# Optimization experiments

Measured on AMD Instinct MI355X. Metric: run time of the kernel, lower is better.

The kernel has to match this reference:

```python
import jax, jax.numpy as jnp
import numpy as np

D_IN = 768      # residual-stream width
D_SAE = 16384   # dictionary size
T = 4           # positions per window
K = 64          # TopK sparsity
PREFIX = (8192, 16384)  # prefix_sum for n_scales=2 even split
B = 1024


def setup_inputs() -> dict:
    key = jax.random.key(0)
    ks = jax.random.split(key, 6)
    x = jax.random.normal(ks[0], (B, T, D_IN), jnp.float32)
    # encoder weight ~ kaiming-uniform scale
    W_enc = jax.random.normal(ks[1], (T, D_IN, D_SAE), jnp.float32) * (1.0 / np.sqrt(D_IN))
    b_enc = jnp.zeros((D_SAE,), jnp.float32)
    # per-scale decoders, row-normalized over (T, d_in) as in _normalize_decoder
    def make_dec(k, prefix):
        W = jax.random.normal(k, (prefix, T, D_IN), jnp.float32)
        norms = jnp.linalg.norm(W.reshape(prefix, -1), axis=1).clip(1e-8)
        return W / norms[:, None, None]
    W_dec0 = make_dec(ks[2], PREFIX[0])
    W_dec1 = make_dec(ks[3], PREFIX[1])
    b_dec0 = jnp.zeros((T, D_IN), jnp.float32)
    b_dec1 = jnp.zeros((T, D_IN), jnp.float32)
    # non-identity per-position prefix permutation (T, d_sae)
    perm_keys = jax.random.split(ks[4], T)
    pos_prefix_perm = jax.vmap(lambda k: jax.random.permutation(k, D_SAE))(perm_keys).astype(jnp.int32)
    return {
        'x': x, 'W_enc': W_enc, 'b_enc': b_enc,
        'W_dec0': W_dec0, 'b_dec0': b_dec0,
        'W_dec1': W_dec1, 'b_dec1': b_dec1,
        'pos_prefix_perm': pos_prefix_perm,
    }


def reference(x, W_enc, b_enc, W_dec0, b_dec0, W_dec1, b_dec1, pos_prefix_perm):
    # ---- encode: pre-activation + per-row TopK + ReLU scatter into sparse code z
    pre = jnp.einsum('btd,tds->bs', x, W_enc) + b_enc            # (B, d_sae)
    vals, idx = jax.lax.top_k(pre, K)                            # (B, K)
    b = pre.shape[0]
    z = jnp.zeros_like(pre).at[jnp.arange(b)[:, None], idx].set(jax.nn.relu(vals))
    # ---- matryoshka per-(position, scale) reconstruction loss
    total = jnp.asarray(0.0, pre.dtype)
    x_hat_full = None
    for W, bd in ((W_dec0, b_dec0), (W_dec1, b_dec1)):
        prefix = W.shape[0]
        # position-dependent permutation gather: z_g[b,t,p] = z[b, perm[t,p]]
        z_g = z[:, pos_prefix_perm[:, :prefix]]                  # (B, T, prefix)
        x_hat = jnp.einsum('btp,ptd->btd', z_g, W) + bd          # (B, T, d_in)
        # sum over t of mean_b sum_d err^2  (== loop over t in the original)
        total = total + jnp.sum(jnp.mean(jnp.sum((x_hat - x) ** 2, axis=-1), axis=0))
        x_hat_full = x_hat
    total = total / (T * 2)  # divide by T * n_scales
    # aux-k loss: freshly initialized module has no dead latents
    # (num_tokens_since_fired starts at 0 << dead_threshold_tokens), so l_auxk == 0.
    return total, x_hat_full, z
```

## Files before the change

### kernel.cpp

```cpp
#include <hip/hip_runtime.h>
#include <hip/hip_bf16.h>
#include <stdint.h>

#define NB    1024
#define NT    4
#define NDIN  768
#define NSAE  16384
#define NK    64
#define KDIM  3072
#define PFX0  8192
#define KT96  96
#define VKD   6144

typedef _Float16 f16x8 __attribute__((ext_vector_type(8)));
typedef _Float16 f16x4 __attribute__((ext_vector_type(4)));
typedef float    f32x4 __attribute__((ext_vector_type(4)));

__device__ __forceinline__ unsigned f2key(float f) {
    union { float f; unsigned u; } cv; cv.f = f;
    unsigned u = cv.u;
    return u ^ ((unsigned)((int)u >> 31) | 0x80000000u);
}

__device__ __forceinline__ void ld16(const void* g, void* l) {
    __builtin_amdgcn_global_load_lds(
        (const __attribute__((address_space(1))) void*)g,
        (__attribute__((address_space(3))) void*)l, 16, 0, 0);
}

__global__ __launch_bounds__(256) void conv_a_kernel(
    const float* __restrict__ A, _Float16* __restrict__ A2)
{
    const int gid = blockIdx.x * 256 + threadIdx.x;
    const int m = gid / (KDIM / 4);
    const int k = (gid % (KDIM / 4)) * 4;
    const float4 v = *(const float4*)(A + (size_t)m * KDIM + k);
    const float vv[4] = { v.x, v.y, v.z, v.w };
    f16x4 h, l;
#pragma unroll
    for (int j = 0; j < 4; ++j) {
        const float sv = vv[j] * 64.f;
        const _Float16 hh = (_Float16)sv;
        h[j] = hh;
        l[j] = (_Float16)(sv - (float)hh);
    }
    const size_t ob = (size_t)m * VKD + (k >> 5) * 64 + (k & 31);
    *(f16x4*)(A2 + ob)      = h;
    *(f16x4*)(A2 + ob + 32) = l;
}

__global__ __launch_bounds__(512, 2) void gemm_f16split_kernel(
    const _Float16* __restrict__ A2, const float* __restrict__ Bsrc,
    const float* __restrict__ bias, float* __restrict__ pre)
{
    __shared__ _Float16 sA[2 * 256 * 64];
    __shared__ float    sB32[2 * 32 * 256];
    const int tid = threadIdx.x;
    const int lane = tid & 63;
    const int wid = tid >> 6;
    const int wm = wid >> 2;
    const int wn = wid & 3;

    const int bid = blockIdx.x;
    const int swz = (bid & 7) * 32 + (bid >> 3);
    const int m0 = (swz & 3) * 256;
    const int n0 = (swz >> 2) * 256;

    const _Float16* pa[4]; const float* pb[4];
    _Float16* da[4]; float* db[4];
#pragma unroll
    for (int r = 0; r < 4; ++r) {
        const int d = tid + r * 512;
        const int rowA = d >> 3;
        const int lsA = (d & 7) ^ (rowA & 7);
        pa[r] = A2 + (size_t)(m0 + rowA) * VKD + lsA * 8;
        da[r] = sA + d * 8;
        const int kB = d >> 6;
        const int slotB = d & 63;
        const int gk = (kB & 7) ^ (((kB >> 3) & 3) << 2);
        pb[r] = Bsrc + (size_t)kB * NSAE + n0 + ((slotB ^ gk) << 2);
        db[r] = sB32 + d * 4;
    }

    const int rl = lane & 15;
    const int qw = lane >> 4;
    const int aoff0 = ((0 + qw) ^ (rl & 7)) * 8 + rl * 64;
    const int aoff1 = ((4 + qw) ^ (rl & 7)) * 8 + rl * 64;

    f32x4 acc[8][4];
#pragma unroll
    for (int mi = 0; mi < 8; ++mi)
#pragma unroll
        for (int ni = 0; ni < 4; ++ni)
            acc[mi][ni] = (f32x4){0.f, 0.f, 0.f, 0.f};

#pragma unroll
    for (int r = 0; r < 4; ++r) { ld16(pa[r], da[r]); ld16(pb[r], db[r]); }

    const size_t KSTRB = (size_t)32 * NSAE;

    for (int kt = 0; kt < KT96; ++kt) {
        const int cbA = (kt & 1) ? 16384 : 0;
        const int nbA = cbA ^ 16384;
        const int cbB = (kt & 1) ? 8192 : 0;
        const int nbB = cbB ^ 8192;
        if (kt + 1 < KT96) {
            const int koA = (kt + 1) * 64;
            const size_t koB = (size_t)(kt + 1) * KSTRB;
#pragma unroll
            for (int r = 0; r < 4; ++r) {
                ld16(pa[r] + koA, da[r] + nbA);
                ld16(pb[r] + koB, db[r] + nbB);
            }
            asm volatile("s_waitcnt vmcnt(8)" ::: "memory");
        } else {
            asm volatile("s_waitcnt vmcnt(0)" ::: "memory");
        }
        __builtin_amdgcn_sched_barrier(0);
        __builtin_amdgcn_s_barrier();
        __builtin_amdgcn_sched_barrier(0);

        __builtin_amdgcn_s_setprio(1);
        f16x8 bf[4][2];
#pragma unroll
        for (int ni = 0; ni < 4; ++ni) {
            const int nslot = wn * 16 + ni * 4 + (rl >> 2);
            const int s0 = nslot ^ (qw << 2);
            const int base = cbB + (qw * 8) * 256 + (rl & 3);
            float fv[8];
#pragma unroll
            for (int j = 0; j < 8; ++j)
                fv[j] = sB32[base + j * 256 + ((s0 ^ j) << 2)];
            f16x8 h, l;
#pragma unroll
            for (int j = 0; j < 8; ++j) {
                const float sv = fv[j] * 64.f;
                const _Float16 hh = (_Float16)sv;
                h[j] = hh;
                l[j] = (_Float16)(sv - (float)hh);
            }
            bf[ni][0] = h;
            bf[ni][1] = l;
        }
#pragma unroll
        for (int h = 0; h < 2; ++h) {
            f16x8 af[4][2];
#pragma unroll
            for (int i = 0; i < 4; ++i) {
                const int ra = cbA + (wm * 128 + (h * 4 + i) * 16) * 64;
                af[i][0] = *(const f16x8*)(sA + ra + aoff0);
                af[i][1] = *(const f16x8*)(sA + ra + aoff1);
            }
#pragma unroll
            for (int i = 0; i < 4; ++i)
#pragma unroll
                for (int ni = 0; ni < 4; ++ni) {
                    acc[h * 4 + i][ni] = __builtin_amdgcn_mfma_f32_16x16x32_f16(af[i][0], bf[ni][0], acc[h * 4 + i][ni], 0, 0, 0);
                    acc[h * 4 + i][ni] = __builtin_amdgcn_mfma_f32_16x16x32_f16(af[i][0], bf[ni][1], acc[h * 4 + i][ni], 0, 0, 0);
                    acc[h * 4 + i][ni] = __builtin_amdgcn_mfma_f32_16x16x32_f16(af[i][1], bf[ni][0], acc[h * 4 + i][ni], 0, 0, 0);
                }
        }
        __builtin_amdgcn_s_setprio(0);
        __builtin_amdgcn_sched_barrier(0);
        __builtin_amdgcn_s_barrier();
    }

    const float c12 = 1.0f / 4096.0f;
    float bv[4];
#pragma unroll
    for (int ni = 0; ni < 4; ++ni) bv[ni] = bias[n0 + wn * 64 + ni * 16 + rl];
#pragma unroll
    for (int mi = 0; mi < 8; ++mi)
#pragma unroll
        for (int ni = 0; ni < 4; ++ni)
#pragma unroll
            for (int r = 0; r < 4; ++r) {
                const int row = m0 + wm * 128 + mi * 16 + qw * 4 + r;
                const int col = n0 + wn * 64 + ni * 16 + rl;
                pre[(size_t)row * NSAE + col] = acc[mi][ni][r] * c12 + bv[ni];
            }
}

__global__ __launch_bounds__(256) void gemm_pre_kernel(
    const float* __restrict__ A, const float* __restrict__ Bm,
    const float* __restrict__ bias, float* __restrict__ pre)
{
    __shared__ float As[16][128];
    __shared__ float Bs[16][128];
    const int bn = blockIdx.x * 128;
    const int bm = blockIdx.y * 128;
    const int tid = threadIdx.x;
    const int tx = tid & 15;
    const int ty = tid >> 4;

    float acc[8][8];
#pragma unroll
    for (int i = 0; i < 8; ++i)
#pragma unroll
        for (int j = 0; j < 8; ++j) acc[i][j] = 0.f;

    for (int k0 = 0; k0 < KDIM; k0 += 16) {
#pragma unroll
        for (int i = 0; i < 2; ++i) {
            const int idx = i * 256 + tid;
            const int r = idx >> 2;
            const int c = (idx & 3) << 2;
            const float4 v = *(const float4*)(A + (size_t)(bm + r) * KDIM + (k0 + c));
            As[c + 0][r] = v.x; As[c + 1][r] = v.y;
            As[c + 2][r] = v.z; As[c + 3][r] = v.w;
        }
#pragma unroll
        for (int i = 0; i < 2; ++i) {
            const int idx = i * 256 + tid;
            const int r = idx >> 5;
            const int c = (idx & 31) << 2;
            *(float4*)(&Bs[r][c]) = *(const float4*)(Bm + (size_t)(k0 + r) * NSAE + (bn + c));
        }
        __syncthreads();
#pragma unroll
        for (int kk = 0; kk < 16; ++kk) {
            const float4 a0 = *(const float4*)(&As[kk][ty * 8]);
            const float4 a1 = *(const float4*)(&As[kk][ty * 8 + 4]);
            const float4 b0 = *(const float4*)(&Bs[kk][tx * 8]);
            const float4 b1 = *(const float4*)(&Bs[kk][tx * 8 + 4]);
            const float av[8] = { a0.x, a0.y, a0.z, a0.w, a1.x, a1.y, a1.z, a1.w };
            const float bv[8] = { b0.x, b0.y, b0.z, b0.w, b1.x, b1.y, b1.z, b1.w };
#pragma unroll
            for (int i = 0; i < 8; ++i)
#pragma unroll
                for (int j = 0; j < 8; ++j)
                    acc[i][j] = fmaf(av[i], bv[j], acc[i][j]);
        }
        __syncthreads();
    }

    float bv8[8];
#pragma unroll
    for (int j = 0; j < 8; ++j) bv8[j] = bias[bn + tx * 8 + j];
#pragma unroll
    for (int i = 0; i < 8; ++i) {
        float4 o0, o1;
        o0.x = acc[i][0] + bv8[0]; o0.y = acc[i][1] + bv8[1];
        o0.z = acc[i][2] + bv8[2]; o0.w = acc[i][3] + bv8[3];
        o1.x = acc[i][4] + bv8[4]; o1.y = acc[i][5] + bv8[5];
        o1.z = acc[i][6] + bv8[6]; o1.w = acc[i][7] + bv8[7];
        const size_t off = (size_t)(bm + ty * 8 + i) * NSAE + bn + tx * 8;
        *(float4*)(pre + off) = o0;
        *(float4*)(pre + off + 4) = o1;
    }
}

__global__ __launch_bounds__(256) void topk_kernel(
    const float* __restrict__ pre,
    int* __restrict__ tk_idx, float* __restrict__ tk_val,
    float* __restrict__ z)
{
    __shared__ unsigned hist[4][256];
    __shared__ int sel[NK];
    __shared__ float sval[NK];
    __shared__ int ties[256];
    __shared__ float tval[256];
    __shared__ unsigned sh_prefix, sh_want, sh_cnt, sh_tiecnt;

    const int b = blockIdx.x;
    const int tid = threadIdx.x;
    const int w = tid >> 6;
    const float* row = pre + (size_t)b * NSAE;
    float* zrow = z + (size_t)b * NSAE;

    if (tid == 0) { sh_prefix = 0u; sh_want = NK; sh_cnt = 0u; sh_tiecnt = 0u; }
    hist[0][tid] = 0u; hist[1][tid] = 0u; hist[2][tid] = 0u; hist[3][tid] = 0u;
    __syncthreads();

    float4 rv[16];
#pragma unroll
    for (int j = 0; j < 16; ++j) {
        const int i = tid * 4 + j * 1024;
        rv[j] = *(const float4*)(row + i);
        *(float4*)(zrow + i) = make_float4(0.f, 0.f, 0.f, 0.f);
        atomicAdd(&hist[w][f2key(rv[j].x) >> 24], 1u);
        atomicAdd(&hist[w][f2key(rv[j].y) >> 24], 1u);
        atomicAdd(&hist[w][f2key(rv[j].z) >> 24], 1u);
        atomicAdd(&hist[w][f2key(rv[j].w) >> 24], 1u);
    }
    __syncthreads();
    hist[0][tid] += hist[1][tid] + hist[2][tid] + hist[3][tid];
    __syncthreads();
    if (tid == 0) {
        unsigned cum = 0u; int bsel = 0;
        for (int bin = 255; bin >= 0; --bin) {
            const unsigned c = hist[0][bin];
            if (cum + c >= NK) { bsel = bin; break; }
            cum += c;
        }
        sh_prefix = ((unsigned)bsel << 24);
        sh_want = NK - cum;
    }
    __syncthreads();

    for (int pass = 1; pass < 4; ++pass) {
        hist[0][tid] = 0u; hist[1][tid] = 0u; hist[2][tid] = 0u; hist[3][tid] = 0u;
        __syncthreads();
        const int shift = 24 - pass * 8;
        const unsigned mask = 0xFFFFFFFFu << (shift + 8);
        const unsigned pfx = sh_prefix;
#pragma unroll
        for (int j = 0; j < 16; ++j) {
            const float fv[4] = { rv[j].x, rv[j].y, rv[j].z, rv[j].w };
#pragma unroll
            for (int q = 0; q < 4; ++q) {
                const unsigned k = f2key(fv[q]);
                if ((k & mask) == pfx) atomicAdd(&hist[w][(k >> shift) & 0xFFu], 1u);
            }
        }
        __syncthreads();
        hist[0][tid] += hist[1][tid] + hist[2][tid] + hist[3][tid];
        __syncthreads();
        if (tid == 0) {
            const unsigned want = sh_want;
            unsigned cum = 0u; int bsel = 0;
            for (int bin = 255; bin >= 0; --bin) {
                const unsigned c = hist[0][bin];
                if (cum + c >= want) { bsel = bin; break; }
                cum += c;
            }
            sh_prefix |= ((unsigned)bsel << shift);
            sh_want = want - cum;
        }
        __syncthreads();
    }

    const unsigned T = sh_prefix;
#pragma unroll
    for (int j = 0; j < 16; ++j) {
        const float fv[4] = { rv[j].x, rv[j].y, rv[j].z, rv[j].w };
#pragma unroll
        for (int q = 0; q < 4; ++q) {
            const unsigned k = f2key(fv[q]);
            if (k > T) {
                const unsigned s = atomicAdd(&sh_cnt, 1u);
                sel[s] = tid * 4 + j * 1024 + q;
                sval[s] = fv[q];
            } else if (k == T) {
                const unsigned s = atomicAdd(&sh_tiecnt, 1u);
                if (s < 256u) { ties[s] = tid * 4 + j * 1024 + q; tval[s] = fv[q]; }
            }
        }
    }
    __syncthreads();
    if (tid == 0) {
        const unsigned tc = sh_tiecnt;
        const int n = (int)(tc < 256u ? tc : 256u);
        for (int a = 1; a < n; ++a) {
            const int v = ties[a]; const float fv = tval[a]; int c = a;
            while (c > 0 && ties[c - 1] > v) {
                ties[c] = ties[c - 1]; tval[c] = tval[c - 1]; --c;
            }
            ties[c] = v; tval[c] = fv;
        }
        const int base = (int)sh_cnt;
        const int want = (int)sh_want;
        for (int j = 0; j < want && j < n; ++j) {
            sel[base + j] = ties[j]; sval[base + j] = tval[j];
        }
    }
    __syncthreads();
    if (tid < NK) {
        const int myi = sel[tid];
        int rank = 0;
#pragma unroll 1
        for (int j = 0; j < NK; ++j) rank += (sel[j] < myi) ? 1 : 0;
        const float v = fmaxf(sval[tid], 0.f);
        tk_idx[b * NK + rank] = myi;
        tk_val[b * NK + rank] = v;
        zrow[myi] = v;
    }
}

__global__ __launch_bounds__(256) void invperm_kernel(
    const int* __restrict__ perm, int* __restrict__ ipos)
{
    const int i = blockIdx.x * 256 + threadIdx.x;
    if (i < NT * NSAE) {
        const int t = i >> 14;
        ipos[t * NSAE + perm[i]] = i & (NSAE - 1);
    }
}

__global__ __launch_bounds__(256) void decode_kernel(
    const float* __restrict__ x,
    const int* __restrict__ tk_idx, const float* __restrict__ tk_val,
    const int* __restrict__ ipos,
    const float* __restrict__ Wd0, const float* __restrict__ bd0,
    const float* __restrict__ Wd1, const float* __restrict__ bd1,
    float* __restrict__ xhat, float* __restrict__ part0, float* __restrict__ part1)
{
    const int gbid = blockIdx.x;
    const int t = gbid >> 10;
    const int b = gbid & (NB - 1);
    const int bt = b * NT + t;
    const int tid = threadIdx.x;

    __shared__ int s_p[NK];
    __shared__ float s_v[NK];
    if (tid < NK) {
        const int s = tk_idx[b * NK + tid];
        s_v[tid] = tk_val[b * NK + tid];
        s_p[tid] = ipos[t * NSAE + s];
    }
    __syncthreads();

    float acc0[3], acc1[3];
#pragma unroll
    for (int r = 0; r < 3; ++r) {
        const int d = tid + 256 * r;
        acc0[r] = bd0[t * NDIN + d];
        acc1[r] = bd1[t * NDIN + d];
    }
    for (int j = 0; j < NK; ++j) {
        const int p = s_p[j];
        const float v = s_v[j];
        const float* w1 = Wd1 + ((size_t)p * NT + t) * NDIN;
#pragma unroll
        for (int r = 0; r < 3; ++r) acc1[r] = fmaf(v, w1[tid + 256 * r], acc1[r]);
        if (p < PFX0) {
            const float* w0 = Wd0 + ((size_t)p * NT + t) * NDIN;
#pragma unroll
            for (int r = 0; r < 3; ++r) acc0[r] = fmaf(v, w0[tid + 256 * r], acc0[r]);
        }
    }

    float e0 = 0.f, e1 = 0.f;
#pragma unroll
    for (int r = 0; r < 3; ++r) {
        const int d = tid + 256 * r;
        const float xv = x[(size_t)bt * NDIN + d];
        const float d0 = acc0[r] - xv;
        const float d1 = acc1[r] - xv;
        e0 = fmaf(d0, d0, e0);
        e1 = fmaf(d1, d1, e1);
        xhat[(size_t)bt * NDIN + d] = acc1[r];
    }

    __shared__ float r0[256];
    __shared__ float r1[256];
    r0[tid] = e0; r1[tid] = e1;
    __syncthreads();
    for (int w = 128; w > 0; w >>= 1) {
        if (tid < w) { r0[tid] += r0[tid + w]; r1[tid] += r1[tid + w]; }
        __syncthreads();
    }
    if (tid == 0) { part0[bt] = r0[0]; part1[bt] = r1[0]; }
}

__global__ __launch_bounds__(256) void reduce_kernel(
    const float* __restrict__ part0, const float* __restrict__ part1,
    float* __restrict__ out_total)
{
    __shared__ double red[256];
    const int tid = threadIdx.x;
    double s = 0.0;
    for (int i = tid; i < NB * NT; i += 256)
        s += (double)part0[i] + (double)part1[i];
    red[tid] = s;
    __syncthreads();
    for (int w = 128; w > 0; w >>= 1) {
        if (tid < w) red[tid] += red[tid + w];
        __syncthreads();
    }
    if (tid == 0) out_total[0] = (float)(red[0] / ((double)NB * (double)(NT * 2)));
}

extern "C" void kernel_launch(void* const* d_in, const int* in_sizes, int n_in,
                              void* d_out, int out_size, void* d_ws, size_t ws_size,
                              hipStream_t stream)
{
    const float* x     = (const float*)d_in[0];
    const float* W_enc = (const float*)d_in[1];
    const float* b_enc = (const float*)d_in[2];
    const float* Wd0   = (const float*)d_in[3];
    const float* bd0   = (const float*)d_in[4];
    const float* Wd1   = (const float*)d_in[5];
    const float* bd1   = (const float*)d_in[6];
    const int*   perm  = (const int*)d_in[7];

    float* out       = (float*)d_out;
    float* out_total = out;
    float* out_xhat  = out + 1;
    float* out_z     = out + 1 + (size_t)NB * NT * NDIN;

    char* ws = (char*)d_ws;
    size_t off = 0;
    float* pre = (float*)(ws + off); off += (size_t)NB * NSAE * sizeof(float);

    const size_t szA2 = (size_t)NB * VKD * sizeof(_Float16);
    _Float16* A2 = (_Float16*)(ws + off);
    const size_t off_splits_end = off + szA2;

    const bool fast = (ws_size >= off_splits_end +
        ((size_t)NB * NK * 8 + (size_t)NT * NSAE * 4 + (size_t)NB * NT * 8));
    size_t tail = fast ? off_splits_end : off;
    int*   tk_idx = (int*)(ws + tail);   tail += (size_t)NB * NK * sizeof(int);
    float* tk_val = (float*)(ws + tail); tail += (size_t)NB * NK * sizeof(float);
    int*   ipos   = (int*)(ws + tail);   tail += (size_t)NT * NSAE * sizeof(int);
    float* part0  = (float*)(ws + tail); tail += (size_t)NB * NT * sizeof(float);
    float* part1  = (float*)(ws + tail);

    if (fast) {
        conv_a_kernel<<<(NB * KDIM) / (256 * 4), 256, 0, stream>>>(x, A2);
        gemm_f16split_kernel<<<256, 512, 0, stream>>>(A2, W_enc, b_enc, pre);
    } else {
        gemm_pre_kernel<<<dim3(NSAE / 128, NB / 128), 256, 0, stream>>>(x, W_enc, b_enc, pre);
    }
    invperm_kernel<<<(NT * NSAE) / 256, 256, 0, stream>>>(perm, ipos);
    topk_kernel<<<NB, 256, 0, stream>>>(pre, tk_idx, tk_val, out_z);
    decode_kernel<<<NB * NT, 256, 0, stream>>>(x, tk_idx, tk_val, ipos,
                                               Wd0, bd0, Wd1, bd1,
                                               out_xhat, part0, part1);
    reduce_kernel<<<1, 256, 0, stream>>>(part0, part1, out_total);
}
```

Before: 593.0 us.

## Convert B tile to split fp16 once per k-step in a shared staging buffer

Instead of every wave converting fp32 B values from shared memory into hi/lo fp16 pairs (redundant across the two M-warps), the block cooperatively converts the single-buffered fp32 B tile once per k-step into a swizzled fp16 tile, which the waves then read as vector fragments. The B fp32 buffer becomes single-buffered, and an extra barrier plus a full vmcnt wait at the end of each iteration are added. This cuts redundant conversion ALU and strided LDS reads, but it serializes global loads with compute more tightly and adds a synchronization per iteration.

```diff
diff --git a/kernel.cpp b/kernel.cpp
--- a/kernel.cpp
+++ b/kernel.cpp
@@ -54,7 +54,8 @@
     const float* __restrict__ bias, float* __restrict__ pre)
 {
     __shared__ _Float16 sA[2 * 256 * 64];
-    __shared__ float    sB32[2 * 32 * 256];
+    __shared__ float    sB32[32 * 256];
+    __shared__ _Float16 sBf[256 * 64];
     const int tid = threadIdx.x;
     const int lane = tid & 63;
     const int wid = tid >> 6;
@@ -77,15 +78,19 @@
         da[r] = sA + d * 8;
         const int kB = d >> 6;
         const int slotB = d & 63;
-        const int gk = (kB & 7) ^ (((kB >> 3) & 3) << 2);
-        pb[r] = Bsrc + (size_t)kB * NSAE + n0 + ((slotB ^ gk) << 2);
+        pb[r] = Bsrc + (size_t)kB * NSAE + n0 + slotB * 4;
         db[r] = sB32 + d * 4;
     }
 
     const int rl = lane & 15;
     const int qw = lane >> 4;
-    const int aoff0 = ((0 + qw) ^ (rl & 7)) * 8 + rl * 64;
-    const int aoff1 = ((4 + qw) ^ (rl & 7)) * 8 + rl * 64;
+    const int off0 = ((0 + qw) ^ (rl & 7)) * 8 + rl * 64;
+    const int off1 = ((4 + qw) ^ (rl & 7)) * 8 + rl * 64;
+
+    const int cvn = tid & 255;
+    const int cvkh = tid >> 8;
+    const int cvsw = cvn & 7;
+    _Float16* const cvout = sBf + cvn * 64;
 
     f32x4 acc[8][4];
 #pragma unroll
@@ -96,51 +101,63 @@
 
 #pragma unroll
     for (int r = 0; r < 4; ++r) { ld16(pa[r], da[r]); ld16(pb[r], db[r]); }
+    asm volatile("s_waitcnt vmcnt(0)" ::: "memory");
+    __builtin_amdgcn_sched_barrier(0);
+    __builtin_amdgcn_s_barrier();
+    __builtin_amdgcn_sched_barrier(0);
 
     const size_t KSTRB = (size_t)32 * NSAE;
 
     for (int kt = 0; kt < KT96; ++kt) {
         const int cbA = (kt & 1) ? 16384 : 0;
         const int nbA = cbA ^ 16384;
-        const int cbB = (kt & 1) ? 8192 : 0;
-        const int nbB = cbB ^ 8192;
+
+        {
+            float v[16];
+#pragma unroll
+            for (int j = 0; j < 16; ++j)
+                v[j] = sB32[(cvkh * 16 + j) * 256 + cvn];
+            f16x8 h0{}, h1{}, l0{}, l1{};
+#pragma unroll
+            for (int j = 0; j < 8; ++j) {
+                const float sv = v[j] * 64.f;
+                const _Float16 hh = (_Float16)sv;
+                h0[j] = hh;
+                l0[j] = (_Float16)(sv - (float)hh);
+            }
+#pragma unroll
+            for (int j = 0; j < 8; ++j) {
+                const float sv = v[8 + j] * 64.f;
+                const _Float16 hh = (_Float16)sv;
+                h1[j] = hh;
+                l1[j] = (_Float16)(sv - (float)hh);
+            }
+            *(f16x8*)(cvout + (((cvkh * 2 + 0) ^ cvsw) * 8)) = h0;
+            *(f16x8*)(cvout + (((cvkh * 2 + 1) ^ cvsw) * 8)) = h1;
+            *(f16x8*)(cvout + (((4 + cvkh * 2 + 0) ^ cvsw) * 8)) = l0;
+            *(f16x8*)(cvout + (((4 + cvkh * 2 + 1) ^ cvsw) * 8)) = l1;
+        }
+        asm volatile("s_waitcnt lgkmcnt(0)" ::: "memory");
+        __builtin_amdgcn_sched_barrier(0);
+        __builtin_amdgcn_s_barrier();
+        __builtin_amdgcn_sched_barrier(0);
+
         if (kt + 1 < KT96) {
             const int koA = (kt + 1) * 64;
             const size_t koB = (size_t)(kt + 1) * KSTRB;
 #pragma unroll
             for (int r = 0; r < 4; ++r) {
                 ld16(pa[r] + koA, da[r] + nbA);
-                ld16(pb[r] + koB, db[r] + nbB);
-            }
-            asm volatile("s_waitcnt vmcnt(8)" ::: "memory");
-        } else {
-            asm volatile("s_waitcnt vmcnt(0)" ::: "memory");
-        }
-        __builtin_amdgcn_sched_barrier(0);
-        __builtin_amdgcn_s_barrier();
-        __builtin_amdgcn_sched_barrier(0);
-
+                ld16(pb[r] + koB, db[r]);
+            }
+        }
         __builtin_amdgcn_s_setprio(1);
         f16x8 bf[4][2];
 #pragma unroll
         for (int ni = 0; ni < 4; ++ni) {
-            const int nslot = wn * 16 + ni * 4 + (rl >> 2);
-            const int s0 = nslot ^ (qw << 2);
-            const int base = cbB + (qw * 8) * 256 + (rl & 3);
-            float fv[8];
-#pragma unroll
-            for (int j = 0; j < 8; ++j)
-                fv[j] = sB32[base + j * 256 + ((s0 ^ j) << 2)];
-            f16x8 h, l;
-#pragma unroll
-            for (int j = 0; j < 8; ++j) {
-                const float sv = fv[j] * 64.f;
-                const _Float16 hh = (_Float16)sv;
-                h[j] = hh;
-                l[j] = (_Float16)(sv - (float)hh);
-            }
-            bf[ni][0] = h;
-            bf[ni][1] = l;
+            const int rb = (wn * 64 + ni * 16) * 64;
+            bf[ni][0] = *(const f16x8*)(sBf + rb + off0);
+            bf[ni][1] = *(const f16x8*)(sBf + rb + off1);
         }
 #pragma unroll
         for (int h = 0; h < 2; ++h) {
@@ -148,8 +165,8 @@
 #pragma unroll
             for (int i = 0; i < 4; ++i) {
                 const int ra = cbA + (wm * 128 + (h * 4 + i) * 16) * 64;
-                af[i][0] = *(const f16x8*)(sA + ra + aoff0);
-                af[i][1] = *(const f16x8*)(sA + ra + aoff1);
+                af[i][0] = *(const f16x8*)(sA + ra + off0);
+                af[i][1] = *(const f16x8*)(sA + ra + off1);
             }
 #pragma unroll
             for (int i = 0; i < 4; ++i)
@@ -162,7 +179,10 @@
         }
         __builtin_amdgcn_s_setprio(0);
         __builtin_amdgcn_sched_barrier(0);
+        asm volatile("s_waitcnt vmcnt(0)" ::: "memory");
+        __builtin_amdgcn_sched_barrier(0);
         __builtin_amdgcn_s_barrier();
+        __builtin_amdgcn_sched_barrier(0);
     }
 
     const float c12 = 1.0f / 4096.0f;
```

Measured after the change: 565.6 us. 1.05x faster.
